# Performance work log

Hardware: AMD Instinct MI355X
Metric: run time of the kernel (lower is better)

Reference implementation:

```python
import jax, jax.numpy as jnp
import numpy as np

B, T, J, C, H = 128, 512, 21, 3, 64


def setup_inputs() -> dict:
    key = jax.random.key(0)
    ks = jax.random.split(key, 14)
    x = jax.random.normal(ks[0], (B, T, J, C), dtype=jnp.float32)
    # Fixed skeleton-like adjacency buffer: symmetric, self-loops, row-normalized.
    A = (jax.random.uniform(ks[1], (J, J)) < 0.15).astype(jnp.float32)
    A = jnp.clip(A + A.T, 0.0, 1.0) + jnp.eye(J, dtype=jnp.float32)
    A = A / A.sum(axis=1, keepdims=True)
    s = 0.05
    W1 = jax.random.normal(ks[2], (H, C), jnp.float32) * s
    b1 = jnp.zeros((H,), jnp.float32)
    W2 = jax.random.normal(ks[3], (H, H), jnp.float32) * s
    b2 = jnp.zeros((H,), jnp.float32)
    Wa = jax.random.normal(ks[4], (1, H), jnp.float32) * s
    ba = jnp.zeros((1,), jnp.float32)
    W_ih = jax.random.normal(ks[5], (3 * H, J * H), jnp.float32) * s
    b_ih = jnp.zeros((3 * H,), jnp.float32)
    W_hh = jax.random.normal(ks[6], (3 * H, H), jnp.float32) * s
    b_hh = jnp.zeros((3 * H,), jnp.float32)
    W_head = jax.random.normal(ks[7], (J * C, H), jnp.float32) * s
    b_head = jnp.zeros((J * C,), jnp.float32)
    return {"x": x, "A": A, "W1": W1, "b1": b1, "W2": W2, "b2": b2,
            "Wa": Wa, "ba": ba, "W_ih": W_ih, "b_ih": b_ih,
            "W_hh": W_hh, "b_hh": b_hh, "W_head": W_head, "b_head": b_head}


def _gcn(A, x, W, b):
    # aggregated = einsum('ij,btjc->btic'); then Linear + ReLU
    agg = jnp.einsum('ij,btjc->btic', A, x)
    return jax.nn.relu(agg @ W.T + b)


def reference(x, A, W1, b1, W2, b2, Wa, ba, W_ih, b_ih, W_hh, b_hh, W_head, b_head):
    h = _gcn(A, x, W1, b1)            # (B,T,J,H)
    h = _gcn(A, h, W2, b2)            # (B,T,J,H)
    # Spatial attention: per-node score, mean over time, softmax over joints
    scores = (h @ Wa.T + ba).mean(axis=1)        # (B,J,1)
    attn = jax.nn.softmax(scores, axis=1)        # (B,J,1)
    h = h * attn[:, None]                        # (B,T,J,H)
    b_, t_, j_, c_ = h.shape
    seq = h.reshape(b_, t_, j_ * c_)             # (B,T,J*H)
    # GRU (PyTorch convention). Precompute input projections outside the scan.
    xproj = seq @ W_ih.T + b_ih                  # (B,T,3H)
    h0 = jnp.zeros((b_, H), xproj.dtype)

    def step(hprev, xp):
        gh = hprev @ W_hh.T + b_hh
        xr, xz, xn = jnp.split(xp, 3, axis=-1)
        hr, hz, hn = jnp.split(gh, 3, axis=-1)
        r = jax.nn.sigmoid(xr + hr)
        z = jax.nn.sigmoid(xz + hz)
        n = jnp.tanh(xn + r * hn)
        hnew = (1.0 - z) * n + z * hprev
        return hnew, None

    hT, _ = jax.lax.scan(step, h0, jnp.swapaxes(xproj, 0, 1))  # last hidden state
    out = hT @ W_head.T + b_head                 # (B, J*C)
    return out, attn.squeeze(-1)
```

## Files before the change

kernel.cpp:

```cpp
#include <hip/hip_runtime.h>
#include <cstdint>
#include <cstddef>

#define NB 128
#define NT 512
#define NJ 21
#define NC 3
#define NH 64
#define JH 1344
#define G3 192
#define OUT0 (NB*NJ*NC)
#define FB 4

typedef __attribute__((ext_vector_type(8))) __bf16 bf16x8;
typedef __attribute__((ext_vector_type(4))) float f32x4;

__device__ __forceinline__ float bf2f(unsigned short u) {
  union { unsigned int i; float f; } v; v.i = ((unsigned int)u) << 16; return v.f;
}
__device__ __forceinline__ unsigned short f2bf(float f) {
  union { float f; unsigned int i; } v; v.f = f;
  unsigned int x = v.i;
  unsigned int lsb = (x >> 16) & 1u;
  x += 0x7fffu + lsb;
  return (unsigned short)(x >> 16);
}
__device__ __forceinline__ unsigned int pk_bf16(float lo, float hi) {
  unsigned int r;
  asm("v_cvt_pk_bf16_f32 %0, %1, %2" : "=v"(r) : "v"(lo), "v"(hi));
  return r;
}
__device__ __forceinline__ unsigned int scale2(unsigned int u, float s) {
  float lo = __uint_as_float(u << 16);
  float hi = __uint_as_float(u & 0xffff0000u);
  return pk_bf16(lo * s, hi * s);
}

__global__ __launch_bounds__(256) void k0_convw(
    const float* __restrict__ W, unsigned short* __restrict__ Wbf) {
  const int ti = blockIdx.x*256 + threadIdx.x;
  const float4 v = ((const float4*)W)[ti];
  uint2 o;
  o.x = (unsigned int)f2bf(v.x) | ((unsigned int)f2bf(v.y) << 16);
  o.y = (unsigned int)f2bf(v.z) | ((unsigned int)f2bf(v.w) << 16);
  ((uint2*)Wbf)[ti] = o;
}

__global__ __launch_bounds__(256, 2) void k1_fused(
    const float* __restrict__ x, const float* __restrict__ A,
    const float* __restrict__ W1, const float* __restrict__ b1,
    const float* __restrict__ W2, const float* __restrict__ b2,
    const float* __restrict__ Wa,
    unsigned short* __restrict__ h2out, float* __restrict__ scorepart) {
  __shared__ unsigned short h1s[FB*32*72];
  __shared__ unsigned short us[FB*64*40];
  __shared__ unsigned short w2s[64*72];
  __shared__ unsigned short adjs[32*40];
  __shared__ unsigned short h2st[FB*NJ*72];
  __shared__ float afs[NJ*NJ];
  __shared__ float xs[4][64];
  __shared__ float ags[4][64];
  __shared__ float spred[4][NJ];

  const int tid = threadIdx.x;
  const int w = tid >> 6, l = tid & 63;
  const int q = l >> 4, r = l & 15;
  const int b = blockIdx.x >> 7, ch = blockIdx.x & 127;
  const int t0 = ch * FB;

  for (int i = tid; i < NJ*NJ; i += 256) afs[i] = A[i];
  for (int i = tid; i < 1024; i += 256) {
    const int ii = i >> 5, jj = i & 31;
    adjs[ii*40 + jj] = (ii < NJ && jj < NJ) ? f2bf(A[ii*NJ + jj]) : (unsigned short)0;
  }
  {
    const int h = tid & 63, qd = tid >> 6;
    const int g0 = qd * 16;
#pragma unroll
    for (int e = 0; e < 16; e += 2) {
      const float v0 = W2[h*64 + g0 + e], v1 = W2[h*64 + g0 + e + 1];
      ((unsigned int*)w2s)[h*36 + ((g0 + e) >> 1)] = pk_bf16(v0, v1);
    }
  }
#pragma unroll
  for (int j = NJ; j < 32; ++j)
    ((unsigned int*)h1s)[(w*32 + j)*36 + (l & 31)] = 0u;

  const float w1r0 = W1[l*3+0], w1r1 = W1[l*3+1], w1r2 = W1[l*3+2];
  const float b1h = b1[l];
  float b2v[4][4], wav[4][4];
#pragma unroll
  for (int mt = 0; mt < 4; ++mt)
#pragma unroll
    for (int rg = 0; rg < 4; ++rg) {
      const int h = mt*16 + q*4 + rg;
      b2v[mt][rg] = b2[h]; wav[mt][rg] = Wa[h];
    }
  __syncthreads();

  {
    const size_t fr = (size_t)(b*NT + t0 + w);
    if (l < NJ*NC) xs[w][l] = x[fr*(NJ*NC) + l];
    if (l < NJ*NC) {
      const int ji = l / 3, c = l - ji*3;
      float s = 0.f;
#pragma unroll
      for (int j = 0; j < NJ; ++j) s += afs[ji*NJ + j] * xs[w][j*3 + c];
      ags[w][l] = s;
    }
#pragma unroll
    for (int j = 0; j < NJ; ++j) {
      float v = b1h + w1r0*ags[w][j*3+0] + w1r1*ags[w][j*3+1] + w1r2*ags[w][j*3+2];
      v = fmaxf(v, 0.f);
      h1s[(w*32 + j)*72 + l] = f2bf(v);
    }
  }
  __syncthreads();

  bf16x8 bw[2][4];
#pragma unroll
  for (int ks = 0; ks < 2; ++ks)
#pragma unroll
    for (int nt = 0; nt < 4; ++nt)
      bw[ks][nt] = *(const bf16x8*)(&w2s[(nt*16 + r)*72 + (ks*4 + q)*8]);
  f32x4 acc1[2][4];
#pragma unroll
  for (int i = 0; i < 2; ++i)
#pragma unroll
    for (int j2 = 0; j2 < 4; ++j2) acc1[i][j2] = (f32x4)0.f;
#pragma unroll
  for (int mti = 0; mti < 2; ++mti) {
    const int row = (w*2 + mti)*16 + r;
#pragma unroll
    for (int ks = 0; ks < 2; ++ks) {
      const bf16x8 af = *(const bf16x8*)(&h1s[row*72 + (ks*4 + q)*8]);
#pragma unroll
      for (int nt = 0; nt < 4; ++nt)
        acc1[mti][nt] = __builtin_amdgcn_mfma_f32_16x16x32_bf16(af, bw[ks][nt], acc1[mti][nt], 0,0,0);
    }
  }
#pragma unroll
  for (int mti = 0; mti < 2; ++mti)
#pragma unroll
    for (int nt = 0; nt < 4; ++nt) {
      const int h = nt*16 + r;
#pragma unroll
      for (int rp = 0; rp < 2; ++rp) {
        const int jp = mti*16 + q*4 + rp*2;
        ((unsigned int*)us)[(w*64 + h)*20 + (jp >> 1)] =
            pk_bf16(acc1[mti][nt][rp*2], acc1[mti][nt][rp*2+1]);
      }
    }
  __syncthreads();

  bf16x8 badj[2];
#pragma unroll
  for (int nt = 0; nt < 2; ++nt)
    badj[nt] = *(const bf16x8*)(&adjs[(nt*16 + r)*40 + q*8]);
  f32x4 acc2[4][2];
#pragma unroll
  for (int i = 0; i < 4; ++i) { acc2[i][0] = (f32x4)0.f; acc2[i][1] = (f32x4)0.f; }
#pragma unroll
  for (int mt = 0; mt < 4; ++mt) {
    const int h = mt*16 + r;
    const bf16x8 af = *(const bf16x8*)(&us[(w*64 + h)*40 + q*8]);
#pragma unroll
    for (int nt = 0; nt < 2; ++nt)
      acc2[mt][nt] = __builtin_amdgcn_mfma_f32_16x16x32_bf16(af, badj[nt], acc2[mt][nt], 0,0,0);
  }
  float sp0 = 0.f, sp1 = 0.f;
#pragma unroll
  for (int nt = 0; nt < 2; ++nt) {
    const int i = nt*16 + r;
    if (i < NJ) {
#pragma unroll
      for (int mt = 0; mt < 4; ++mt)
#pragma unroll
        for (int rp = 0; rp < 2; ++rp) {
          const int h0 = mt*16 + q*4 + rp*2;
          const float v0 = fmaxf(acc2[mt][nt][rp*2]   + b2v[mt][rp*2],   0.f);
          const float v1 = fmaxf(acc2[mt][nt][rp*2+1] + b2v[mt][rp*2+1], 0.f);
          if (nt == 0) sp0 += v0*wav[mt][rp*2] + v1*wav[mt][rp*2+1];
          else         sp1 += v0*wav[mt][rp*2] + v1*wav[mt][rp*2+1];
          ((unsigned int*)h2st)[(w*NJ + i)*36 + (h0 >> 1)] = pk_bf16(v0, v1);
        }
    }
  }
  sp0 += __shfl_xor(sp0, 16); sp0 += __shfl_xor(sp0, 32);
  sp1 += __shfl_xor(sp1, 16); sp1 += __shfl_xor(sp1, 32);
  if (l < 16) spred[w][l] = sp0;
  if (l < 5)  spred[w][16 + l] = sp1;
  __syncthreads();

  if (tid < NJ)
    scorepart[((size_t)b*128 + ch)*NJ + tid] =
      spred[0][tid] + spred[1][tid] + spred[2][tid] + spred[3][tid];

  const size_t gbase = (size_t)(b*NT + t0) * JH;
  for (int cid = tid; cid < FB*NJ*8; cid += 256) {
    const int f = cid / (NJ*8), rem = cid - f*(NJ*8);
    const int i = rem >> 3, p = rem & 7;
    const uint4 v = *(const uint4*)(&h2st[(f*NJ + i)*72 + p*8]);
    *(uint4*)(&h2out[gbase + (size_t)f*JH + i*64 + p*8]) = v;
  }
}

__global__ __launch_bounds__(64) void k2_attn(
    const float* __restrict__ scorepart, float* __restrict__ attn,
    float* __restrict__ out_attn) {
  __shared__ float ss[NJ];
  const int b = blockIdx.x, tid = threadIdx.x;
  if (tid < NJ) {
    float s = 0.f;
    for (int ch = 0; ch < 128; ++ch) s += scorepart[(b*128 + ch)*NJ + tid];
    ss[tid] = s * (1.0f/NT);
  }
  __syncthreads();
  float m = -1e30f;
  for (int j = 0; j < NJ; ++j) m = fmaxf(m, ss[j]);
  float sum = 0.f;
  for (int j = 0; j < NJ; ++j) sum += expf(ss[j] - m);
  if (tid < NJ) {
    float a = expf(ss[tid] - m) / sum;
    attn[b*NJ + tid] = a;
    out_attn[b*NJ + tid] = a;
  }
}

__global__ __launch_bounds__(256, 2) void k3_xproj_mfma(
    const unsigned short* __restrict__ h2, const unsigned short* __restrict__ Wbf,
    const float* __restrict__ b_ih, const float* __restrict__ attn,
    float* __restrict__ xproj) {
  __shared__ unsigned short Abuf[2][128*32];
  __shared__ unsigned short Bbuf[2][192*32];
  const int tid = threadIdx.x;
  const int w = tid >> 6, l = tid & 63;
  const int lq = l >> 4, lr = l & 15;
  const int blk = blockIdx.x;
  const int b = blk >> 2;
  const int t0 = (blk & 3) << 7;
  const int wm = w >> 1, wn = w & 1;

  const unsigned short* gA[2]; int ldsA[2];
#pragma unroll
  for (int i = 0; i < 2; ++i) {
    const int lc = tid*2 + i, rr = lc >> 2, j = lc & 3;
    gA[i] = h2 + (size_t)(b*NT + t0 + rr)*JH + j*8;
    ldsA[i] = rr*32 + ((j ^ ((rr>>1)&3)) << 3);
  }
  const unsigned short* gB[3]; int ldsB[3];
#pragma unroll
  for (int i = 0; i < 3; ++i) {
    const int lc = tid + 256*i, g = lc >> 2, j = lc & 3;
    gB[i] = Wbf + (size_t)g*JH + j*8;
    ldsB[i] = g*32 + ((j ^ ((g>>1)&3)) << 3);
  }
  int aoff[4], boff[6];
#pragma unroll
  for (int mt = 0; mt < 4; ++mt) {
    const int row = wm*64 + mt*16 + lr;
    aoff[mt] = row*32 + ((lq ^ ((row>>1)&3)) << 3);
  }
#pragma unroll
  for (int nt = 0; nt < 6; ++nt) {
    const int g = wn*96 + nt*16 + lr;
    boff[nt] = g*32 + ((lq ^ ((g>>1)&3)) << 3);
  }

  f32x4 acc[4][6];
#pragma unroll
  for (int mt = 0; mt < 4; ++mt)
#pragma unroll
    for (int nt = 0; nt < 6; ++nt) acc[mt][nt] = (f32x4)0.f;

  {
    const float s = attn[b*NJ + 0];
#pragma unroll
    for (int i = 0; i < 2; ++i)
      *(uint4*)(&Abuf[0][ldsA[i]]) = *(const uint4*)(gA[i]);
#pragma unroll
    for (int i = 0; i < 3; ++i) {
      uint4 v = *(const uint4*)(gB[i]);
      v.x = scale2(v.x, s); v.y = scale2(v.y, s);
      v.z = scale2(v.z, s); v.w = scale2(v.w, s);
      *(uint4*)(&Bbuf[0][ldsB[i]]) = v;
    }
  }
  __syncthreads();

  for (int ks = 0; ks < 42; ++ks) {
    const int cur = ks & 1;
    uint4 av0, av1, bv0, bv1, bv2;
    if (ks < 41) {
      const int kk = (ks+1)*32;
      av0 = *(const uint4*)(gA[0] + kk);
      av1 = *(const uint4*)(gA[1] + kk);
      bv0 = *(const uint4*)(gB[0] + kk);
      bv1 = *(const uint4*)(gB[1] + kk);
      bv2 = *(const uint4*)(gB[2] + kk);
    }
    bf16x8 af[4], bfr[6];
#pragma unroll
    for (int mt = 0; mt < 4; ++mt) af[mt] = *(const bf16x8*)(&Abuf[cur][aoff[mt]]);
#pragma unroll
    for (int nt = 0; nt < 6; ++nt) bfr[nt] = *(const bf16x8*)(&Bbuf[cur][boff[nt]]);
#pragma unroll
    for (int mt = 0; mt < 4; ++mt)
#pragma unroll
      for (int nt = 0; nt < 6; ++nt)
        acc[mt][nt] = __builtin_amdgcn_mfma_f32_16x16x32_bf16(af[mt], bfr[nt], acc[mt][nt], 0, 0, 0);
    if (ks < 41) {
      const float s = attn[b*NJ + ((ks+1) >> 1)];
      *(uint4*)(&Abuf[cur^1][ldsA[0]]) = av0;
      *(uint4*)(&Abuf[cur^1][ldsA[1]]) = av1;
      uint4 v;
      v = bv0; v.x = scale2(v.x, s); v.y = scale2(v.y, s); v.z = scale2(v.z, s); v.w = scale2(v.w, s);
      *(uint4*)(&Bbuf[cur^1][ldsB[0]]) = v;
      v = bv1; v.x = scale2(v.x, s); v.y = scale2(v.y, s); v.z = scale2(v.z, s); v.w = scale2(v.w, s);
      *(uint4*)(&Bbuf[cur^1][ldsB[1]]) = v;
      v = bv2; v.x = scale2(v.x, s); v.y = scale2(v.y, s); v.z = scale2(v.z, s); v.w = scale2(v.w, s);
      *(uint4*)(&Bbuf[cur^1][ldsB[2]]) = v;
    }
    __syncthreads();
  }

  float bias[6];
#pragma unroll
  for (int nt = 0; nt < 6; ++nt) bias[nt] = b_ih[wn*96 + nt*16 + lr];
#pragma unroll
  for (int mt = 0; mt < 4; ++mt)
#pragma unroll
    for (int nt = 0; nt < 6; ++nt) {
      const int g = wn*96 + nt*16 + lr;
      const int trow = t0 + wm*64 + mt*16 + lq*4;
      float4 o;
      o.x = acc[mt][nt][0] + bias[nt];
      o.y = acc[mt][nt][1] + bias[nt];
      o.z = acc[mt][nt][2] + bias[nt];
      o.w = acc[mt][nt][3] + bias[nt];
      *(float4*)(&xproj[(size_t)(b*G3 + g)*NT + trow]) = o;
    }
}

__global__ __launch_bounds__(512, 1) void k4_gru_mfma(
    const float* __restrict__ xproj, const float* __restrict__ W_hh,
    const float* __restrict__ b_hh, float* __restrict__ hT) {
  __shared__ __align__(16) unsigned short hb[2][2][16*72];
  const int tid = threadIdx.x;
  const int w = tid >> 6, l = tid & 63, q = l >> 4, r15 = l & 15;
  const int b0 = blockIdx.x * 16;

  for (int i = tid; i < 2*2*16*72; i += 512) (&hb[0][0][0])[i] = 0;

  bf16x8 afr[2][2];
  int chv[2]; float br_[2], bz_[2], bn_[2];
#pragma unroll
  for (int i = 0; i < 2; ++i) {
    const int mt = 2*w + i;
    const int row = mt*16 + r15;
    const int chs = row >> 2, gate = row & 3;
#pragma unroll
    for (int ks = 0; ks < 2; ++ks) {
      union { bf16x8 v; unsigned int u[4]; } tu;
      if (gate < 3) {
        const float* src = W_hh + (size_t)(gate*NH + chs)*NH + ks*32 + q*8;
        const float4 a = *(const float4*)(src);
        const float4 b = *(const float4*)(src + 4);
        tu.u[0] = pk_bf16(a.x, a.y); tu.u[1] = pk_bf16(a.z, a.w);
        tu.u[2] = pk_bf16(b.x, b.y); tu.u[3] = pk_bf16(b.z, b.w);
      } else {
        tu.u[0]=0u; tu.u[1]=0u; tu.u[2]=0u; tu.u[3]=0u;
      }
      afr[i][ks] = tu.v;
    }
    chv[i] = mt*4 + q;
    br_[i] = b_hh[chv[i]]; bz_[i] = b_hh[NH + chv[i]]; bn_[i] = b_hh[2*NH + chv[i]];
  }

  const float* xrow[2][3];
#pragma unroll
  for (int i = 0; i < 2; ++i)
#pragma unroll
    for (int e = 0; e < 3; ++e)
      xrow[i][e] = xproj + (size_t)((b0 + r15)*G3 + e*NH + chv[i]) * NT;

  f32x4 cur[2][3], nxt[2][3];
#pragma unroll
  for (int i = 0; i < 2; ++i)
#pragma unroll
    for (int e = 0; e < 3; ++e) cur[i][e] = *(const f32x4*)(xrow[i][e]);

  float hprev[2] = {0.f, 0.f};
  __syncthreads();

  for (int tg = 0; tg < NT; tg += 4) {
    if (tg + 4 < NT) {
#pragma unroll
      for (int i = 0; i < 2; ++i)
#pragma unroll
        for (int e = 0; e < 3; ++e) nxt[i][e] = *(const f32x4*)(xrow[i][e] + tg + 4);
    }
#pragma unroll
    for (int p = 0; p < 4; ++p) {
      const int rb = p & 1, wb = rb ^ 1;
      const bf16x8 bhi0 = *(const bf16x8*)(&hb[rb][0][r15*72 + q*8]);
      const bf16x8 bhi1 = *(const bf16x8*)(&hb[rb][0][r15*72 + 32 + q*8]);
      const bf16x8 blo0 = *(const bf16x8*)(&hb[rb][1][r15*72 + q*8]);
      const bf16x8 blo1 = *(const bf16x8*)(&hb[rb][1][r15*72 + 32 + q*8]);
#pragma unroll
      for (int i = 0; i < 2; ++i) {
        f32x4 acc = (f32x4)0.f;
        acc = __builtin_amdgcn_mfma_f32_16x16x32_bf16(afr[i][0], blo0, acc, 0,0,0);
        acc = __builtin_amdgcn_mfma_f32_16x16x32_bf16(afr[i][1], blo1, acc, 0,0,0);
        acc = __builtin_amdgcn_mfma_f32_16x16x32_bf16(afr[i][0], bhi0, acc, 0,0,0);
        acc = __builtin_amdgcn_mfma_f32_16x16x32_bf16(afr[i][1], bhi1, acc, 0,0,0);
        const float xr = cur[i][0][p], xz = cur[i][1][p], xn = cur[i][2][p];
        const float hr = acc[0] + br_[i];
        const float hz = acc[1] + bz_[i];
        const float hn = acc[2] + bn_[i];
        const float rr = __builtin_amdgcn_rcpf(1.f + __expf(-(xr + hr)));
        const float zz = __builtin_amdgcn_rcpf(1.f + __expf(-(xz + hz)));
        const float nx = xn + rr*hn;
        const float nn = 2.f*__builtin_amdgcn_rcpf(1.f + __expf(-2.f*nx)) - 1.f;
        const float h = (1.f - zz)*nn + zz*hprev[i];
        hprev[i] = h;
        const unsigned short hi16 = f2bf(h);
        const unsigned short lo16 = f2bf(h - bf2f(hi16));
        hb[wb][0][r15*72 + chv[i]] = hi16;
        hb[wb][1][r15*72 + chv[i]] = lo16;
      }
      __syncthreads();
    }
#pragma unroll
    for (int i = 0; i < 2; ++i)
#pragma unroll
      for (int e = 0; e < 3; ++e) cur[i][e] = nxt[i][e];
  }

#pragma unroll
  for (int i = 0; i < 2; ++i)
    hT[(size_t)(b0 + r15)*NH + chv[i]] = hprev[i];
}

__global__ __launch_bounds__(256) void k5_head(
    const float* __restrict__ hT, const float* __restrict__ W_head,
    const float* __restrict__ b_head, float* __restrict__ out) {
  const int idx = blockIdx.x*256 + threadIdx.x;
  if (idx >= NB*63) return;
  const int b = idx / 63, rr = idx % 63;
  const float* hv = hT + b*NH;
  const float* wr = W_head + rr*NH;
  float acc = b_head[rr];
#pragma unroll
  for (int k = 0; k < NH; ++k) acc += hv[k]*wr[k];
  out[idx] = acc;
}

extern "C" void kernel_launch(void* const* d_in, const int* in_sizes, int n_in,
                              void* d_out, int out_size, void* d_ws, size_t ws_size,
                              hipStream_t stream) {
  const float* x      = (const float*)d_in[0];
  const float* A      = (const float*)d_in[1];
  const float* W1     = (const float*)d_in[2];
  const float* b1     = (const float*)d_in[3];
  const float* W2     = (const float*)d_in[4];
  const float* b2     = (const float*)d_in[5];
  const float* Wa     = (const float*)d_in[6];
  const float* W_ih   = (const float*)d_in[8];
  const float* b_ih   = (const float*)d_in[9];
  const float* W_hh   = (const float*)d_in[10];
  const float* b_hh   = (const float*)d_in[11];
  const float* W_head = (const float*)d_in[12];
  const float* b_head = (const float*)d_in[13];
  float* out = (float*)d_out;

  char* ws = (char*)d_ws;
  size_t off = 0;
  unsigned short* h2 = (unsigned short*)(ws + off); off += (size_t)NB*NT*JH*2;
  float* scorepart   = (float*)(ws + off);          off += (size_t)NB*128*NJ*4;
  float* attn        = (float*)(ws + off);          off += (size_t)NB*NJ*4;
  off = (off + 15) & ~(size_t)15;
  float* xproj       = (float*)(ws + off);          off += (size_t)NB*NT*G3*4;
  float* hT          = (float*)(ws + off);          off += (size_t)NB*NH*4;
  off = (off + 15) & ~(size_t)15;
  unsigned short* Wbf = (unsigned short*)(ws + off); off += (size_t)G3*JH*2;

  k0_convw<<<dim3(252),       256, 0, stream>>>(W_ih, Wbf);
  k1_fused<<<dim3(NB*128),    256, 0, stream>>>(x, A, W1, b1, W2, b2, Wa, h2, scorepart);
  k2_attn<<<dim3(NB),          64, 0, stream>>>(scorepart, attn, out + OUT0);
  k3_xproj_mfma<<<dim3(512),  256, 0, stream>>>(h2, Wbf, b_ih, attn, xproj);
  k4_gru_mfma<<<dim3(8),      512, 0, stream>>>(xproj, W_hh, b_hh, hT);
  k5_head<<<dim3((NB*63 + 255)/256), 256, 0, stream>>>(hT, W_head, b_head, out);
}
```

Before: 605.0 us.

## Drop hi/lo bf16 split of GRU hidden state and pack channel writes

The GRU recurrence previously kept the hidden state as a hi+lo bf16 pair and ran four MFMAs per tile to approximate fp32 precision. Now it stores a single bf16 copy, halving the MFMAs and LDS reads per step. It also remaps channels so each lane owns two adjacent channels, which lets it write them with one packed 32-bit LDS store, and it interleaves the two independent MFMA chains. This shortens the serial per-step critical path, but hidden-state precision drops to plain bf16, so error can build up over the 512 steps.

```diff
diff --git a/kernel.cpp b/kernel.cpp
--- a/kernel.cpp
+++ b/kernel.cpp
@@ -345,25 +345,25 @@
 __global__ __launch_bounds__(512, 1) void k4_gru_mfma(
     const float* __restrict__ xproj, const float* __restrict__ W_hh,
     const float* __restrict__ b_hh, float* __restrict__ hT) {
-  __shared__ __align__(16) unsigned short hb[2][2][16*72];
+  __shared__ __align__(16) unsigned short hb[2][16*72];
   const int tid = threadIdx.x;
   const int w = tid >> 6, l = tid & 63, q = l >> 4, r15 = l & 15;
   const int b0 = blockIdx.x * 16;
 
-  for (int i = tid; i < 2*2*16*72; i += 512) (&hb[0][0][0])[i] = 0;
+  for (int i = tid; i < 2*16*36; i += 512) ((unsigned int*)hb)[i] = 0u;
 
   bf16x8 afr[2][2];
   int chv[2]; float br_[2], bz_[2], bn_[2];
 #pragma unroll
   for (int i = 0; i < 2; ++i) {
     const int mt = 2*w + i;
-    const int row = mt*16 + r15;
-    const int chs = row >> 2, gate = row & 3;
+    const int gate = r15 & 3;
+    const int cha = 8*(mt >> 1) + 2*(r15 >> 2) + (mt & 1);
 #pragma unroll
     for (int ks = 0; ks < 2; ++ks) {
       union { bf16x8 v; unsigned int u[4]; } tu;
       if (gate < 3) {
-        const float* src = W_hh + (size_t)(gate*NH + chs)*NH + ks*32 + q*8;
+        const float* src = W_hh + (size_t)(gate*NH + cha)*NH + ks*32 + q*8;
         const float4 a = *(const float4*)(src);
         const float4 b = *(const float4*)(src + 4);
         tu.u[0] = pk_bf16(a.x, a.y); tu.u[1] = pk_bf16(a.z, a.w);
@@ -373,7 +373,7 @@
       }
       afr[i][ks] = tu.v;
     }
-    chv[i] = mt*4 + q;
+    chv[i] = 8*w + 2*q + i;
     br_[i] = b_hh[chv[i]]; bz_[i] = b_hh[NH + chv[i]]; bn_[i] = b_hh[2*NH + chv[i]];
   }
 
@@ -403,32 +403,29 @@
 #pragma unroll
     for (int p = 0; p < 4; ++p) {
       const int rb = p & 1, wb = rb ^ 1;
-      const bf16x8 bhi0 = *(const bf16x8*)(&hb[rb][0][r15*72 + q*8]);
-      const bf16x8 bhi1 = *(const bf16x8*)(&hb[rb][0][r15*72 + 32 + q*8]);
-      const bf16x8 blo0 = *(const bf16x8*)(&hb[rb][1][r15*72 + q*8]);
-      const bf16x8 blo1 = *(const bf16x8*)(&hb[rb][1][r15*72 + 32 + q*8]);
+      const bf16x8 bh0 = *(const bf16x8*)(&hb[rb][r15*72 + q*8]);
+      const bf16x8 bh1 = *(const bf16x8*)(&hb[rb][r15*72 + 32 + q*8]);
+      f32x4 acc[2];
+      acc[0] = (f32x4)0.f; acc[1] = (f32x4)0.f;
+      acc[0] = __builtin_amdgcn_mfma_f32_16x16x32_bf16(afr[0][0], bh0, acc[0], 0,0,0);
+      acc[1] = __builtin_amdgcn_mfma_f32_16x16x32_bf16(afr[1][0], bh0, acc[1], 0,0,0);
+      acc[0] = __builtin_amdgcn_mfma_f32_16x16x32_bf16(afr[0][1], bh1, acc[0], 0,0,0);
+      acc[1] = __builtin_amdgcn_mfma_f32_16x16x32_bf16(afr[1][1], bh1, acc[1], 0,0,0);
+      float hnew[2];
 #pragma unroll
       for (int i = 0; i < 2; ++i) {
-        f32x4 acc = (f32x4)0.f;
-        acc = __builtin_amdgcn_mfma_f32_16x16x32_bf16(afr[i][0], blo0, acc, 0,0,0);
-        acc = __builtin_amdgcn_mfma_f32_16x16x32_bf16(afr[i][1], blo1, acc, 0,0,0);
-        acc = __builtin_amdgcn_mfma_f32_16x16x32_bf16(afr[i][0], bhi0, acc, 0,0,0);
-        acc = __builtin_amdgcn_mfma_f32_16x16x32_bf16(afr[i][1], bhi1, acc, 0,0,0);
         const float xr = cur[i][0][p], xz = cur[i][1][p], xn = cur[i][2][p];
-        const float hr = acc[0] + br_[i];
-        const float hz = acc[1] + bz_[i];
-        const float hn = acc[2] + bn_[i];
+        const float hr = acc[i][0] + br_[i];
+        const float hz = acc[i][1] + bz_[i];
+        const float hn = acc[i][2] + bn_[i];
         const float rr = __builtin_amdgcn_rcpf(1.f + __expf(-(xr + hr)));
         const float zz = __builtin_amdgcn_rcpf(1.f + __expf(-(xz + hz)));
         const float nx = xn + rr*hn;
         const float nn = 2.f*__builtin_amdgcn_rcpf(1.f + __expf(-2.f*nx)) - 1.f;
-        const float h = (1.f - zz)*nn + zz*hprev[i];
-        hprev[i] = h;
-        const unsigned short hi16 = f2bf(h);
-        const unsigned short lo16 = f2bf(h - bf2f(hi16));
-        hb[wb][0][r15*72 + chv[i]] = hi16;
-        hb[wb][1][r15*72 + chv[i]] = lo16;
+        hnew[i] = (1.f - zz)*nn + zz*hprev[i];
+        hprev[i] = hnew[i];
       }
+      ((unsigned int*)&hb[wb][0])[r15*36 + 4*w + q] = pk_bf16(hnew[0], hnew[1]);
       __syncthreads();
     }
 #pragma unroll
```

Measured after the change: 561.6 us. -7.2%, faster.
